# Performance work log

Hardware: AMD Instinct MI355X
Metric: run time of the kernel (lower is better)

The kernel has to match this reference:

```python
import jax, jax.numpy as jnp
import numpy as np

B, N, K = 8, 2048, 20
EMB = 1024


def _knn(x, k):
    # x: (B, C, N) -> indices of k nearest neighbors (B, N, k) by negative sq. distance
    xx = jnp.sum(x * x, axis=1)                      # (B, N)
    inner = jnp.einsum('bcn,bcm->bnm', x, x)         # (B, N, N)
    neg_d = 2.0 * inner - xx[:, :, None] - xx[:, None, :]
    return jax.lax.top_k(neg_d, k)[1]


def _graph_feature(x, idx):
    # x: (B, C, N), idx: (B, N, k) -> (B, 2C, N, k) = concat(neighbor - center, center)
    nb = jnp.take_along_axis(x[:, :, None, :], idx[:, None, :, :], axis=3)  # (B,C,N,k)
    xc = x[:, :, :, None]
    return jnp.concatenate([nb - xc, jnp.broadcast_to(xc, nb.shape)], axis=1)


def _cbl2(e, W, s, b):
    # 1x1 Conv2d (no bias) + BatchNorm(eval, folded to affine) + LeakyReLU(0.2)
    y = jnp.einsum('oc,bcnk->bonk', W, e)
    return jax.nn.leaky_relu(y * s[None, :, None, None] + b[None, :, None, None], 0.2)


def _cbl1(x, W, s, b):
    y = jnp.einsum('oc,bcn->bon', W, x)
    return jax.nn.leaky_relu(y * s[None, :, None] + b[None, :, None], 0.2)


def setup_inputs() -> dict:
    key = jax.random.key(0)
    ks = jax.random.split(key, 64)
    i = [0]

    def nk():
        i[0] += 1
        return ks[i[0]]

    def w(o, c):
        return jax.random.normal(nk(), (o, c), jnp.float32) * np.float32(1.0 / np.sqrt(c))

    def sb(c):
        s = jax.random.uniform(nk(), (c,), jnp.float32, 0.5, 1.5)
        b = jax.random.normal(nk(), (c,), jnp.float32) * 0.1
        return s, b

    inp = {'x': jax.random.normal(nk(), (B, 9, N), jnp.float32)}
    inp['w1a'] = w(64, 18);  inp['s1a'], inp['b1a'] = sb(64)
    inp['w1b'] = w(64, 64);  inp['s1b'], inp['b1b'] = sb(64)
    inp['w2a'] = w(64, 128); inp['s2a'], inp['b2a'] = sb(64)
    inp['w2b'] = w(64, 64);  inp['s2b'], inp['b2b'] = sb(64)
    inp['w3'] = w(64, 128);  inp['s3'], inp['b3'] = sb(64)
    inp['w4'] = w(EMB, 192); inp['s4'], inp['b4'] = sb(EMB)
    inp['w5a'] = w(512, EMB + 192); inp['s5a'], inp['b5a'] = sb(512)
    inp['w5b'] = w(256, 512); inp['s5b'], inp['b5b'] = sb(256)
    inp['w6'] = w(13, 256)
    return inp


def reference(x, w1a, s1a, b1a, w1b, s1b, b1b, w2a, s2a, b2a, w2b, s2b, b2b,
              w3, s3, b3, w4, s4, b4, w5a, s5a, b5a, w5b, s5b, b5b, w6):
    # EdgeConv block 1 (knn on xyz channels 6:9)
    e = _graph_feature(x, _knn(x[:, 6:], K))          # (B, 18, N, K)
    e = _cbl2(_cbl2(e, w1a, s1a, b1a), w1b, s1b, b1b)
    x1 = e.max(axis=-1)                               # (B, 64, N)
    # EdgeConv block 2
    e = _graph_feature(x1, _knn(x1, K))               # (B, 128, N, K)
    e = _cbl2(_cbl2(e, w2a, s2a, b2a), w2b, s2b, b2b)
    x2 = e.max(axis=-1)
    # EdgeConv block 3
    e = _graph_feature(x2, _knn(x2, K))
    e = _cbl2(e, w3, s3, b3)
    x3 = e.max(axis=-1)

    xc = jnp.concatenate([x1, x2, x3], axis=1)        # (B, 192, N)
    x4 = _cbl1(xc, w4, s4, b4)                        # (B, EMB, N)
    g = jnp.broadcast_to(x4.max(axis=-1, keepdims=True), (B, EMB, N))
    h = jnp.concatenate([g, x1, x2, x3], axis=1)      # (B, EMB+192, N)
    h = _cbl1(_cbl1(h, w5a, s5a, b5a), w5b, s5b, b5b)
    # dropout in eval mode == identity
    return jnp.einsum('oc,bcn->bon', w6, h)           # (B, 13, N)
```

## Files before the change

kernel.cpp:

```cpp
#include <hip/hip_runtime.h>
#include <cstddef>
#include <cstdint>

namespace {

constexpr int NBATCH = 8;
constexpr int NPTS = 2048;
constexpr int KNN = 20;

__device__ __forceinline__ float lrelu(float v) { return fmaxf(v, 0.2f * v); }

template <int C>
__global__ __launch_bounds__(256) void knn_kernel(const float* __restrict__ x, int chStride,
                                                  int bStride, int* __restrict__ idxOut) {
  constexpr int CP = (C + 3) & ~3;
  constexpr int MT = 128;
  constexpr int ROWS = 32;
  constexpr int RPW = 8;
  constexpr int DS = MT + 4;
  constexpr int NT = NPTS / MT;

  __shared__ float qt[ROWS * CP];
  __shared__ float xt[CP * MT];
  __shared__ float dist[ROWS * DS];

  const int tid = threadIdx.x;
  const int lane = tid & 63;
  const int wv = tid >> 6;
  const int r0 = wv * RPW;
  const int b = blockIdx.x / (NPTS / ROWS);
  const int n0 = (blockIdx.x % (NPTS / ROWS)) * ROWS;
  const float* xb = x + (size_t)b * bStride;

  for (int t = tid; t < ROWS * CP; t += 256) {
    int r = t / CP, c = t % CP;
    qt[r * CP + c] = (c < C) ? xb[(size_t)c * chStride + n0 + r] : 0.f;
  }
  __syncthreads();

  float xn[RPW];
#pragma unroll
  for (int r = 0; r < RPW; ++r) {
    float s = 0.f;
#pragma unroll
    for (int cb = 0; cb < CP; cb += 4) {
      float4 qv = *(const float4*)&qt[(r0 + r) * CP + cb];
      s = fmaf(qv.x, qv.x, s);
      s = fmaf(qv.y, qv.y, s);
      s = fmaf(qv.z, qv.z, s);
      s = fmaf(qv.w, qv.w, s);
    }
    xn[r] = s;
  }

  const int srow = tid >> 3;
  const int ssub = tid & 7;
  double lv[KNN];
#pragma unroll
  for (int s = 0; s < KNN; ++s) lv[s] = -1.0;

#pragma unroll 1
  for (int mt = 0; mt < NT; ++mt) {
    __syncthreads();
    {
      const float4 z4 = make_float4(0.f, 0.f, 0.f, 0.f);
      for (int t = tid; t < CP * MT / 4; t += 256) {
        int f = t * 4;
        int c = f >> 7, m = f & (MT - 1);
        *(float4*)&xt[f] =
            (c < C) ? *(const float4*)&xb[(size_t)c * chStride + mt * MT + m] : z4;
      }
    }
    __syncthreads();

    float acc0[RPW], acc1[RPW];
    float xm0 = 0.f, xm1 = 0.f;
#pragma unroll
    for (int r = 0; r < RPW; ++r) { acc0[r] = 0.f; acc1[r] = 0.f; }
#pragma unroll 1
    for (int cb = 0; cb < CP; cb += 4) {
      float x00 = xt[(cb + 0) * MT + lane];
      float x01 = xt[(cb + 1) * MT + lane];
      float x02 = xt[(cb + 2) * MT + lane];
      float x03 = xt[(cb + 3) * MT + lane];
      float x10 = xt[(cb + 0) * MT + 64 + lane];
      float x11 = xt[(cb + 1) * MT + 64 + lane];
      float x12 = xt[(cb + 2) * MT + 64 + lane];
      float x13 = xt[(cb + 3) * MT + 64 + lane];
      xm0 = fmaf(x00, x00, xm0);
      xm0 = fmaf(x01, x01, xm0);
      xm0 = fmaf(x02, x02, xm0);
      xm0 = fmaf(x03, x03, xm0);
      xm1 = fmaf(x10, x10, xm1);
      xm1 = fmaf(x11, x11, xm1);
      xm1 = fmaf(x12, x12, xm1);
      xm1 = fmaf(x13, x13, xm1);
#pragma unroll
      for (int r = 0; r < RPW; ++r) {
        float4 qv = *(const float4*)&qt[(r0 + r) * CP + cb];
        acc0[r] = fmaf(qv.x, x00, acc0[r]);
        acc0[r] = fmaf(qv.y, x01, acc0[r]);
        acc0[r] = fmaf(qv.z, x02, acc0[r]);
        acc0[r] = fmaf(qv.w, x03, acc0[r]);
        acc1[r] = fmaf(qv.x, x10, acc1[r]);
        acc1[r] = fmaf(qv.y, x11, acc1[r]);
        acc1[r] = fmaf(qv.z, x12, acc1[r]);
        acc1[r] = fmaf(qv.w, x13, acc1[r]);
      }
    }
#pragma unroll
    for (int r = 0; r < RPW; ++r) {
      dist[(r0 + r) * DS + lane] = 2.f * acc0[r] - xn[r] - xm0;
      dist[(r0 + r) * DS + 64 + lane] = 2.f * acc1[r] - xn[r] - xm1;
    }

#pragma unroll 4
    for (int j = 0; j < MT / 8; ++j) {
      float val = dist[srow * DS + j * 8 + ssub];
      int gidx = mt * MT + j * 8 + ssub;
      unsigned int u = __float_as_uint(val);
      u ^= (unsigned int)(((int)u) >> 31) | 0x80000000u;
      unsigned long long key =
          ((unsigned long long)u << 30) | ((unsigned long long)(2047 - gidx) << 19);
      double kd = __longlong_as_double((long long)key);
#pragma unroll
      for (int s = 0; s < KNN - 1; ++s) lv[s] = fmin(lv[s + 1], fmax(lv[s], kd));
      lv[KNN - 1] = fmax(lv[KNN - 1], kd);
    }
  }

  int* op = idxOut + ((size_t)b * NPTS + n0 + srow) * KNN;
#pragma unroll 1
  for (int round = 0; round < KNN; ++round) {
    double bv = lv[KNN - 1];
    bv = fmax(bv, __shfl_xor(bv, 1));
    bv = fmax(bv, __shfl_xor(bv, 2));
    bv = fmax(bv, __shfl_xor(bv, 4));
    if (lv[KNN - 1] == bv) {
#pragma unroll
      for (int s = KNN - 1; s > 0; --s) lv[s] = lv[s - 1];
      lv[0] = -1.0;
    }
    if (ssub == 0)
      op[round] =
          2047 - (int)((unsigned long long)(__double_as_longlong(bv) >> 19) & 0x7FFull);
  }
}

template <int C>
__global__ __launch_bounds__(256) __attribute__((amdgpu_waves_per_eu(4, 4))) void
pointconv_kernel(const float* __restrict__ x, int bStride, const float* __restrict__ W,
                 float* __restrict__ znb, float* __restrict__ base) {
  const int blk = blockIdx.x;
  const int b = blk >> 5;
  const int nc = blk & 31;
  const int nl = threadIdx.x & 63;
  const int q = __builtin_amdgcn_readfirstlane(threadIdx.x >> 6);
  const int n = nc * 64 + nl;
  const float* xb = x + (size_t)b * bStride;

  float fz[16], fb[16];
#pragma unroll
  for (int t = 0; t < 16; ++t) { fz[t] = 0.f; fb[t] = 0.f; }
#pragma unroll 4
  for (int c = 0; c < C; ++c) {
    float xv = xb[(size_t)c * NPTS + n];
#pragma unroll
    for (int t = 0; t < 16; ++t) {
      float w0 = W[(q * 16 + t) * 2 * C + c];
      float w1 = W[(q * 16 + t) * 2 * C + C + c];
      fz[t] = fmaf(w0, xv, fz[t]);
      fb[t] = fmaf(w1 - w0, xv, fb[t]);
    }
  }
  const size_t o0 = ((size_t)(b * NPTS + n)) * 64 + q * 16;
#pragma unroll
  for (int t = 0; t < 16; t += 4)
    *(float4*)&znb[o0 + t] = make_float4(fz[t], fz[t + 1], fz[t + 2], fz[t + 3]);
#pragma unroll
  for (int t = 0; t < 16; t += 4)
    *(float4*)&base[o0 + t] = make_float4(fb[t], fb[t + 1], fb[t + 2], fb[t + 3]);
}

template <bool TWO>
__global__ __launch_bounds__(256) __attribute__((amdgpu_waves_per_eu(2, 4))) void edge_kernel(
    const float* __restrict__ znb, const float* __restrict__ base,
    const int* __restrict__ idx, const float* __restrict__ s1, const float* __restrict__ b1,
    const float* __restrict__ W2, const float* __restrict__ s2, const float* __restrict__ b2,
    float* __restrict__ xout) {
  __shared__ float baseS[12][64];
  const int tid = threadIdx.x;
  const int gp0 = blockIdx.x * 12;

  for (int t = tid; t < 12 * 64; t += 256) {
    int p = t >> 6, cp = t & 63;
    int gpt = gp0 + p;
    baseS[p][cp] = (gpt < NBATCH * NPTS) ? base[(size_t)gpt * 64 + cp] : 0.f;
  }
  __syncthreads();

  const int lane = tid & 63;
  const int wv = __builtin_amdgcn_readfirstlane(tid >> 6);
  int p = lane / 20;
  const int k = lane - p * 20;
  const bool pact = (p < 3);
  if (!pact) p = 2;
  const int pl = wv * 3 + p;
  const int gpt = gp0 + pl;
  const bool act = pact && (gpt < NBATCH * NPTS);
  const int gptc = (gpt < NBATCH * NPTS) ? gpt : (NBATCH * NPTS - 1);
  const int bb = gptc >> 11;
  const int nn = gptc & (NPTS - 1);
  const int m = idx[(size_t)gptc * KNN + k];
  const float* zg = znb + ((size_t)bb * NPTS + m) * 64;

  float y1[64];
#pragma unroll
  for (int c4 = 0; c4 < 64; c4 += 4) {
    float4 zv = *(const float4*)&zg[c4];
    float4 bv = *(const float4*)&baseS[pl][c4];
    y1[c4 + 0] = zv.x + bv.x;
    y1[c4 + 1] = zv.y + bv.y;
    y1[c4 + 2] = zv.z + bv.z;
    y1[c4 + 3] = zv.w + bv.w;
  }
#pragma unroll
  for (int cp = 0; cp < 64; ++cp) y1[cp] = lrelu(fmaf(y1[cp], s1[cp], b1[cp]));

  if constexpr (TWO) {
#pragma unroll 2
    for (int o2 = 0; o2 < 64; ++o2) {
      float a = 0.f;
#pragma unroll
      for (int c = 0; c < 64; ++c) a = fmaf(W2[o2 * 64 + c], y1[c], a);
      float z = lrelu(fmaf(a, s2[o2], b2[o2]));
#pragma unroll
      for (int off = 1; off < 32; off <<= 1) {
        float ov = __shfl_down(z, off);
        if (k + off < KNN) z = fmaxf(z, ov);
      }
      if (act && k == 0) xout[((size_t)bb * 64 + o2) * NPTS + nn] = z;
    }
  } else {
#pragma unroll 2
    for (int o2 = 0; o2 < 64; ++o2) {
      float z = y1[o2];
#pragma unroll
      for (int off = 1; off < 32; off <<= 1) {
        float ov = __shfl_down(z, off);
        if (k + off < KNN) z = fmaxf(z, ov);
      }
      if (act && k == 0) xout[((size_t)bb * 64 + o2) * NPTS + nn] = z;
    }
  }
}

__global__ __launch_bounds__(256) void x4max_kernel(const float* __restrict__ x1,
                                                    const float* __restrict__ x2,
                                                    const float* __restrict__ x3,
                                                    const float* __restrict__ W4,
                                                    const float* __restrict__ s4,
                                                    const float* __restrict__ b4,
                                                    float* __restrict__ pmax) {
  const int blk = blockIdx.x;
  const int b = blk >> 10;
  const int oc = (blk >> 5) & 31;
  const int nc = blk & 31;
  const int nl = threadIdx.x & 63;
  const int q = __builtin_amdgcn_readfirstlane(threadIdx.x >> 6);
  const int n = nc * 64 + nl;
  const float* xA = x1 + (size_t)b * 64 * NPTS;
  const float* xB = x2 + (size_t)b * 64 * NPTS;
  const float* xC = x3 + (size_t)b * 64 * NPTS;
  const float* wq = W4 + (size_t)(oc * 32 + q * 8) * 192;

  float f[8];
#pragma unroll
  for (int t = 0; t < 8; ++t) f[t] = 0.f;
#pragma unroll 2
  for (int cb = 0; cb < 64; cb += 4) {
    float xv0 = xA[(size_t)(cb + 0) * NPTS + n];
    float xv1 = xA[(size_t)(cb + 1) * NPTS + n];
    float xv2 = xA[(size_t)(cb + 2) * NPTS + n];
    float xv3 = xA[(size_t)(cb + 3) * NPTS + n];
#pragma unroll
    for (int t = 0; t < 8; ++t) {
      float4 wv = *(const float4*)&wq[(size_t)t * 192 + cb];
      f[t] = fmaf(wv.x, xv0, f[t]);
      f[t] = fmaf(wv.y, xv1, f[t]);
      f[t] = fmaf(wv.z, xv2, f[t]);
      f[t] = fmaf(wv.w, xv3, f[t]);
    }
  }
#pragma unroll 2
  for (int cb = 0; cb < 64; cb += 4) {
    float xv0 = xB[(size_t)(cb + 0) * NPTS + n];
    float xv1 = xB[(size_t)(cb + 1) * NPTS + n];
    float xv2 = xB[(size_t)(cb + 2) * NPTS + n];
    float xv3 = xB[(size_t)(cb + 3) * NPTS + n];
#pragma unroll
    for (int t = 0; t < 8; ++t) {
      float4 wv = *(const float4*)&wq[(size_t)t * 192 + 64 + cb];
      f[t] = fmaf(wv.x, xv0, f[t]);
      f[t] = fmaf(wv.y, xv1, f[t]);
      f[t] = fmaf(wv.z, xv2, f[t]);
      f[t] = fmaf(wv.w, xv3, f[t]);
    }
  }
#pragma unroll 2
  for (int cb = 0; cb < 64; cb += 4) {
    float xv0 = xC[(size_t)(cb + 0) * NPTS + n];
    float xv1 = xC[(size_t)(cb + 1) * NPTS + n];
    float xv2 = xC[(size_t)(cb + 2) * NPTS + n];
    float xv3 = xC[(size_t)(cb + 3) * NPTS + n];
#pragma unroll
    for (int t = 0; t < 8; ++t) {
      float4 wv = *(const float4*)&wq[(size_t)t * 192 + 128 + cb];
      f[t] = fmaf(wv.x, xv0, f[t]);
      f[t] = fmaf(wv.y, xv1, f[t]);
      f[t] = fmaf(wv.z, xv2, f[t]);
      f[t] = fmaf(wv.w, xv3, f[t]);
    }
  }
#pragma unroll
  for (int t = 0; t < 8; ++t) {
    const int o = oc * 32 + q * 8 + t;
    float v = lrelu(fmaf(f[t], s4[o], b4[o]));
#pragma unroll
    for (int off = 32; off; off >>= 1) v = fmaxf(v, __shfl_down(v, off));
    if (nl == 0) pmax[(size_t)(b * 1024 + o) * 32 + nc] = v;
  }
}

__global__ __launch_bounds__(256) void gmax_kernel(const float* __restrict__ pmax,
                                                   float* __restrict__ g) {
  int i = blockIdx.x * 256 + threadIdx.x;
  if (i >= NBATCH * 1024) return;
  float v = -__builtin_inff();
#pragma unroll
  for (int j = 0; j < 32; ++j) v = fmaxf(v, pmax[(size_t)i * 32 + j]);
  g[i] = v;
}

__global__ __launch_bounds__(256) void t5a_kernel(const float* __restrict__ g,
                                                  const float* __restrict__ w5a,
                                                  float* __restrict__ t5a) {
  const int task = blockIdx.x * 4 + (threadIdx.x >> 6);
  const int lane = threadIdx.x & 63;
  const int b = task >> 9;
  const int o5 = task & 511;
  float acc = 0.f;
  for (int c = lane; c < 1024; c += 64) acc = fmaf(w5a[(size_t)o5 * 1216 + c], g[b * 1024 + c], acc);
#pragma unroll
  for (int off = 32; off; off >>= 1) acc += __shfl_down(acc, off);
  if (lane == 0) t5a[task] = acc;
}

__global__ __launch_bounds__(256) void h1_kernel(const float* __restrict__ x1,
                                                 const float* __restrict__ x2,
                                                 const float* __restrict__ x3,
                                                 const float* __restrict__ t5a,
                                                 const float* __restrict__ w5a,
                                                 const float* __restrict__ s5a,
                                                 const float* __restrict__ b5a,
                                                 float* __restrict__ h1) {
  const int blk = blockIdx.x;
  const int b = blk >> 9;
  const int oc = (blk >> 5) & 15;
  const int nc = blk & 31;
  const int nl = threadIdx.x & 63;
  const int q = __builtin_amdgcn_readfirstlane(threadIdx.x >> 6);
  const int n = nc * 64 + nl;
  const int o0 = oc * 32 + q * 8;
  const float* xA = x1 + (size_t)b * 64 * NPTS;
  const float* xB = x2 + (size_t)b * 64 * NPTS;
  const float* xC = x3 + (size_t)b * 64 * NPTS;
  const float* wq = w5a + (size_t)o0 * 1216 + 1024;

  float f[8];
#pragma unroll
  for (int t = 0; t < 8; ++t) f[t] = t5a[b * 512 + o0 + t];
#pragma unroll 2
  for (int cb = 0; cb < 64; cb += 4) {
    float xv0 = xA[(size_t)(cb + 0) * NPTS + n];
    float xv1 = xA[(size_t)(cb + 1) * NPTS + n];
    float xv2 = xA[(size_t)(cb + 2) * NPTS + n];
    float xv3 = xA[(size_t)(cb + 3) * NPTS + n];
#pragma unroll
    for (int t = 0; t < 8; ++t) {
      float4 wv = *(const float4*)&wq[(size_t)t * 1216 + cb];
      f[t] = fmaf(wv.x, xv0, f[t]);
      f[t] = fmaf(wv.y, xv1, f[t]);
      f[t] = fmaf(wv.z, xv2, f[t]);
      f[t] = fmaf(wv.w, xv3, f[t]);
    }
  }
#pragma unroll 2
  for (int cb = 0; cb < 64; cb += 4) {
    float xv0 = xB[(size_t)(cb + 0) * NPTS + n];
    float xv1 = xB[(size_t)(cb + 1) * NPTS + n];
    float xv2 = xB[(size_t)(cb + 2) * NPTS + n];
    float xv3 = xB[(size_t)(cb + 3) * NPTS + n];
#pragma unroll
    for (int t = 0; t < 8; ++t) {
      float4 wv = *(const float4*)&wq[(size_t)t * 1216 + 64 + cb];
      f[t] = fmaf(wv.x, xv0, f[t]);
      f[t] = fmaf(wv.y, xv1, f[t]);
      f[t] = fmaf(wv.z, xv2, f[t]);
      f[t] = fmaf(wv.w, xv3, f[t]);
    }
  }
#pragma unroll 2
  for (int cb = 0; cb < 64; cb += 4) {
    float xv0 = xC[(size_t)(cb + 0) * NPTS + n];
    float xv1 = xC[(size_t)(cb + 1) * NPTS + n];
    float xv2 = xC[(size_t)(cb + 2) * NPTS + n];
    float xv3 = xC[(size_t)(cb + 3) * NPTS + n];
#pragma unroll
    for (int t = 0; t < 8; ++t) {
      float4 wv = *(const float4*)&wq[(size_t)t * 1216 + 128 + cb];
      f[t] = fmaf(wv.x, xv0, f[t]);
      f[t] = fmaf(wv.y, xv1, f[t]);
      f[t] = fmaf(wv.z, xv2, f[t]);
      f[t] = fmaf(wv.w, xv3, f[t]);
    }
  }
#pragma unroll
  for (int t = 0; t < 8; ++t) {
    const int o = o0 + t;
    h1[((size_t)b * 512 + o) * NPTS + n] = lrelu(fmaf(f[t], s5a[o], b5a[o]));
  }
}

__global__ __launch_bounds__(256) void h2_kernel(const float* __restrict__ h1,
                                                 const float* __restrict__ w5b,
                                                 const float* __restrict__ s5b,
                                                 const float* __restrict__ b5b,
                                                 float* __restrict__ h2) {
  const int blk = blockIdx.x;
  const int b = blk >> 8;
  const int oc = (blk >> 5) & 7;
  const int nc = blk & 31;
  const int nl = threadIdx.x & 63;
  const int q = __builtin_amdgcn_readfirstlane(threadIdx.x >> 6);
  const int n = nc * 64 + nl;
  const int o0 = oc * 32 + q * 8;
  const float* hb = h1 + (size_t)b * 512 * NPTS;
  const float* wq = w5b + (size_t)o0 * 512;

  float f[8];
#pragma unroll
  for (int t = 0; t < 8; ++t) f[t] = 0.f;
#pragma unroll 2
  for (int cb = 0; cb < 512; cb += 4) {
    float xv0 = hb[(size_t)(cb + 0) * NPTS + n];
    float xv1 = hb[(size_t)(cb + 1) * NPTS + n];
    float xv2 = hb[(size_t)(cb + 2) * NPTS + n];
    float xv3 = hb[(size_t)(cb + 3) * NPTS + n];
#pragma unroll
    for (int t = 0; t < 8; ++t) {
      float4 wv = *(const float4*)&wq[(size_t)t * 512 + cb];
      f[t] = fmaf(wv.x, xv0, f[t]);
      f[t] = fmaf(wv.y, xv1, f[t]);
      f[t] = fmaf(wv.z, xv2, f[t]);
      f[t] = fmaf(wv.w, xv3, f[t]);
    }
  }
#pragma unroll
  for (int t = 0; t < 8; ++t) {
    const int o = o0 + t;
    h2[((size_t)b * 256 + o) * NPTS + n] = lrelu(fmaf(f[t], s5b[o], b5b[o]));
  }
}

__global__ __launch_bounds__(256) void out_kernel(const float* __restrict__ h2,
                                                  const float* __restrict__ w6,
                                                  float* __restrict__ out) {
  const int blk = blockIdx.x;
  const int b = blk >> 3;
  const int nc = blk & 7;
  const int n = nc * 256 + threadIdx.x;
  const float* hb = h2 + (size_t)b * 256 * NPTS;

  float f[13];
#pragma unroll
  for (int o = 0; o < 13; ++o) f[o] = 0.f;
#pragma unroll 2
  for (int c = 0; c < 256; ++c) {
    float hv = hb[(size_t)c * NPTS + n];
#pragma unroll
    for (int o = 0; o < 13; ++o) f[o] = fmaf(w6[o * 256 + c], hv, f[o]);
  }
#pragma unroll
  for (int o = 0; o < 13; ++o) out[((size_t)b * 13 + o) * NPTS + n] = f[o];
}

}

extern "C" void kernel_launch(void* const* d_in, const int* in_sizes, int n_in, void* d_out,
                              int out_size, void* d_ws, size_t ws_size, hipStream_t stream) {
  (void)in_sizes; (void)n_in; (void)out_size;
  const float* x = (const float*)d_in[0];
  const float* w1a = (const float*)d_in[1];
  const float* s1a = (const float*)d_in[2];
  const float* b1a = (const float*)d_in[3];
  const float* w1b = (const float*)d_in[4];
  const float* s1b = (const float*)d_in[5];
  const float* b1b = (const float*)d_in[6];
  const float* w2a = (const float*)d_in[7];
  const float* s2a = (const float*)d_in[8];
  const float* b2a = (const float*)d_in[9];
  const float* w2b = (const float*)d_in[10];
  const float* s2b = (const float*)d_in[11];
  const float* b2b = (const float*)d_in[12];
  const float* w3 = (const float*)d_in[13];
  const float* s3 = (const float*)d_in[14];
  const float* b3 = (const float*)d_in[15];
  const float* w4 = (const float*)d_in[16];
  const float* s4 = (const float*)d_in[17];
  const float* b4 = (const float*)d_in[18];
  const float* w5a = (const float*)d_in[19];
  const float* s5a = (const float*)d_in[20];
  const float* b5a = (const float*)d_in[21];
  const float* w5b = (const float*)d_in[22];
  const float* s5b = (const float*)d_in[23];
  const float* b5b = (const float*)d_in[24];
  const float* w6 = (const float*)d_in[25];
  float* out = (float*)d_out;

  char* wsp = (char*)d_ws;
  size_t off = 0;
  auto alloc = [&](size_t bytes) -> void* {
    void* p = wsp + off;
    off += (bytes + 255) & ~(size_t)255;
    return p;
  };
  int* idx1 = (int*)alloc((size_t)NBATCH * NPTS * KNN * 4);
  int* idx2 = (int*)alloc((size_t)NBATCH * NPTS * KNN * 4);
  int* idx3 = (int*)alloc((size_t)NBATCH * NPTS * KNN * 4);
  float* x1 = (float*)alloc((size_t)NBATCH * 64 * NPTS * 4);
  float* x2 = (float*)alloc((size_t)NBATCH * 64 * NPTS * 4);
  float* x3 = (float*)alloc((size_t)NBATCH * 64 * NPTS * 4);
  float* znbBuf = (float*)alloc((size_t)NBATCH * NPTS * 64 * 4);
  float* baseBuf = (float*)alloc((size_t)NBATCH * NPTS * 64 * 4);
  float* pmaxb = (float*)alloc((size_t)NBATCH * 1024 * 32 * 4);
  float* g = (float*)alloc((size_t)NBATCH * 1024 * 4);
  float* t5a = (float*)alloc((size_t)NBATCH * 512 * 4);
  float* h1 = (float*)alloc((size_t)NBATCH * 512 * NPTS * 4);
  float* h2 = (float*)alloc((size_t)NBATCH * 256 * NPTS * 4);

  if (off > ws_size) return;

  const int knnGrid = NBATCH * NPTS / 32;
  const int ecGrid = (NBATCH * NPTS + 11) / 12;
  const int pcGrid = NBATCH * 32;

  knn_kernel<3><<<knnGrid, 256, 0, stream>>>(x + 6 * NPTS, NPTS, 9 * NPTS, idx1);
  pointconv_kernel<9><<<pcGrid, 256, 0, stream>>>(x, 9 * NPTS, w1a, znbBuf, baseBuf);
  edge_kernel<true><<<ecGrid, 256, 0, stream>>>(znbBuf, baseBuf, idx1, s1a, b1a, w1b, s1b, b1b,
                                                x1);
  knn_kernel<64><<<knnGrid, 256, 0, stream>>>(x1, NPTS, 64 * NPTS, idx2);
  pointconv_kernel<64><<<pcGrid, 256, 0, stream>>>(x1, 64 * NPTS, w2a, znbBuf, baseBuf);
  edge_kernel<true><<<ecGrid, 256, 0, stream>>>(znbBuf, baseBuf, idx2, s2a, b2a, w2b, s2b, b2b,
                                                x2);
  knn_kernel<64><<<knnGrid, 256, 0, stream>>>(x2, NPTS, 64 * NPTS, idx3);
  pointconv_kernel<64><<<pcGrid, 256, 0, stream>>>(x2, 64 * NPTS, w3, znbBuf, baseBuf);
  edge_kernel<false><<<ecGrid, 256, 0, stream>>>(znbBuf, baseBuf, idx3, s3, b3, nullptr, nullptr,
                                                 nullptr, x3);
  x4max_kernel<<<8192, 256, 0, stream>>>(x1, x2, x3, w4, s4, b4, pmaxb);
  gmax_kernel<<<32, 256, 0, stream>>>(pmaxb, g);
  t5a_kernel<<<1024, 256, 0, stream>>>(g, w5a, t5a);
  h1_kernel<<<4096, 256, 0, stream>>>(x1, x2, x3, t5a, w5a, s5a, b5a, h1);
  h2_kernel<<<2048, 256, 0, stream>>>(h1, w5b, s5b, b5b, h2);
  out_kernel<<<64, 256, 0, stream>>>(h2, w6, out);
}
```

Measured before the change: 1.086 ms.

## Shrink KNN tile to 16 query rows and split each row's top-k across 16 lanes

The KNN kernel now processes 16 query rows per block with 64-candidate tiles, and each row's running top-k list is split across 16 lanes instead of 8. This doubles the grid and halves the serial sorted-insertion chain each thread runs per candidate, which looks like the dominant cost. An extra shuffle stage is added to the final merge. The candidate index key is now built by decrementing a precomputed value rather than recomputed per element. In exchange, the distance tile is smaller, so there are more tile loads and syncs per candidate and less reuse of loaded candidates across query rows.

```diff
diff --git a/kernel.cpp b/kernel.cpp
--- a/kernel.cpp
+++ b/kernel.cpp
@@ -14,10 +14,11 @@
 __global__ __launch_bounds__(256) void knn_kernel(const float* __restrict__ x, int chStride,
                                                   int bStride, int* __restrict__ idxOut) {
   constexpr int CP = (C + 3) & ~3;
-  constexpr int MT = 128;
-  constexpr int ROWS = 32;
-  constexpr int RPW = 8;
-  constexpr int DS = MT + 4;
+  constexpr int MT = 64;
+  constexpr int ROWS = 16;
+  constexpr int RPW = 4;
+  constexpr int LPR = 16;
+  constexpr int DS = 72;
   constexpr int NT = NPTS / MT;
 
   __shared__ float qt[ROWS * CP];
@@ -53,11 +54,13 @@
     xn[r] = s;
   }
 
-  const int srow = tid >> 3;
-  const int ssub = tid & 7;
+  const int srow = tid >> 4;
+  const int ssub = tid & 15;
   double lv[KNN];
 #pragma unroll
   for (int s = 0; s < KNN; ++s) lv[s] = -1.0;
+
+  unsigned long long ib = (unsigned long long)(2047 - ssub) << 19;
 
 #pragma unroll 1
   for (int mt = 0; mt < NT; ++mt) {
@@ -66,63 +69,47 @@
       const float4 z4 = make_float4(0.f, 0.f, 0.f, 0.f);
       for (int t = tid; t < CP * MT / 4; t += 256) {
         int f = t * 4;
-        int c = f >> 7, m = f & (MT - 1);
+        int c = f >> 6, m = f & (MT - 1);
         *(float4*)&xt[f] =
             (c < C) ? *(const float4*)&xb[(size_t)c * chStride + mt * MT + m] : z4;
       }
     }
     __syncthreads();
 
-    float acc0[RPW], acc1[RPW];
-    float xm0 = 0.f, xm1 = 0.f;
-#pragma unroll
-    for (int r = 0; r < RPW; ++r) { acc0[r] = 0.f; acc1[r] = 0.f; }
+    float acc[RPW];
+    float xm = 0.f;
+#pragma unroll
+    for (int r = 0; r < RPW; ++r) acc[r] = 0.f;
 #pragma unroll 1
     for (int cb = 0; cb < CP; cb += 4) {
-      float x00 = xt[(cb + 0) * MT + lane];
-      float x01 = xt[(cb + 1) * MT + lane];
-      float x02 = xt[(cb + 2) * MT + lane];
-      float x03 = xt[(cb + 3) * MT + lane];
-      float x10 = xt[(cb + 0) * MT + 64 + lane];
-      float x11 = xt[(cb + 1) * MT + 64 + lane];
-      float x12 = xt[(cb + 2) * MT + 64 + lane];
-      float x13 = xt[(cb + 3) * MT + 64 + lane];
-      xm0 = fmaf(x00, x00, xm0);
-      xm0 = fmaf(x01, x01, xm0);
-      xm0 = fmaf(x02, x02, xm0);
-      xm0 = fmaf(x03, x03, xm0);
-      xm1 = fmaf(x10, x10, xm1);
-      xm1 = fmaf(x11, x11, xm1);
-      xm1 = fmaf(x12, x12, xm1);
-      xm1 = fmaf(x13, x13, xm1);
+      float x0 = xt[(cb + 0) * MT + lane];
+      float x1 = xt[(cb + 1) * MT + lane];
+      float x2 = xt[(cb + 2) * MT + lane];
+      float x3 = xt[(cb + 3) * MT + lane];
+      xm = fmaf(x0, x0, xm);
+      xm = fmaf(x1, x1, xm);
+      xm = fmaf(x2, x2, xm);
+      xm = fmaf(x3, x3, xm);
 #pragma unroll
       for (int r = 0; r < RPW; ++r) {
         float4 qv = *(const float4*)&qt[(r0 + r) * CP + cb];
-        acc0[r] = fmaf(qv.x, x00, acc0[r]);
-        acc0[r] = fmaf(qv.y, x01, acc0[r]);
-        acc0[r] = fmaf(qv.z, x02, acc0[r]);
-        acc0[r] = fmaf(qv.w, x03, acc0[r]);
-        acc1[r] = fmaf(qv.x, x10, acc1[r]);
-        acc1[r] = fmaf(qv.y, x11, acc1[r]);
-        acc1[r] = fmaf(qv.z, x12, acc1[r]);
-        acc1[r] = fmaf(qv.w, x13, acc1[r]);
+        acc[r] = fmaf(qv.x, x0, acc[r]);
+        acc[r] = fmaf(qv.y, x1, acc[r]);
+        acc[r] = fmaf(qv.z, x2, acc[r]);
+        acc[r] = fmaf(qv.w, x3, acc[r]);
       }
     }
 #pragma unroll
-    for (int r = 0; r < RPW; ++r) {
-      dist[(r0 + r) * DS + lane] = 2.f * acc0[r] - xn[r] - xm0;
-      dist[(r0 + r) * DS + 64 + lane] = 2.f * acc1[r] - xn[r] - xm1;
-    }
-
-#pragma unroll 4
-    for (int j = 0; j < MT / 8; ++j) {
-      float val = dist[srow * DS + j * 8 + ssub];
-      int gidx = mt * MT + j * 8 + ssub;
+    for (int r = 0; r < RPW; ++r)
+      dist[(r0 + r) * DS + lane] = 2.f * acc[r] - xn[r] - xm;
+
+#pragma unroll
+    for (int j = 0; j < MT / LPR; ++j) {
+      float val = dist[srow * DS + j * LPR + ssub];
       unsigned int u = __float_as_uint(val);
       u ^= (unsigned int)(((int)u) >> 31) | 0x80000000u;
-      unsigned long long key =
-          ((unsigned long long)u << 30) | ((unsigned long long)(2047 - gidx) << 19);
-      double kd = __longlong_as_double((long long)key);
+      double kd = __longlong_as_double((long long)(((unsigned long long)u << 30) | ib));
+      ib -= (unsigned long long)LPR << 19;
 #pragma unroll
       for (int s = 0; s < KNN - 1; ++s) lv[s] = fmin(lv[s + 1], fmax(lv[s], kd));
       lv[KNN - 1] = fmax(lv[KNN - 1], kd);
@@ -136,6 +123,7 @@
     bv = fmax(bv, __shfl_xor(bv, 1));
     bv = fmax(bv, __shfl_xor(bv, 2));
     bv = fmax(bv, __shfl_xor(bv, 4));
+    bv = fmax(bv, __shfl_xor(bv, 8));
     if (lv[KNN - 1] == bv) {
 #pragma unroll
       for (int s = KNN - 1; s > 0; --s) lv[s] = lv[s - 1];
@@ -551,7 +539,7 @@
 
   if (off > ws_size) return;
 
-  const int knnGrid = NBATCH * NPTS / 32;
+  const int knnGrid = NBATCH * NPTS / 16;
   const int ecGrid = (NBATCH * NPTS + 11) / 12;
   const int pcGrid = NBATCH * 32;
 
```

Result: slower. 1.150 ms (+5.9%).
